# Kernel optimization log

Hardware: AMD Instinct MI355X
Metric: run time of the kernel (lower is better)

The kernel has to match this reference:

```python
import jax, jax.numpy as jnp
import numpy as np

ALPHA = 0.2  # LeakyReLU negative slope
NEG_INF = -1.0e12


def setup_inputs() -> dict:
    key = jax.random.key(0)
    ks = jax.random.split(key, 8)
    N, F, D, H, M, Q = 4096, 512, 64, 4, 2, 128
    x = jax.random.normal(ks[0], (N, F), dtype=jnp.float32)
    adj = jax.random.randint(ks[1], (M, N, N), 0, 2, dtype=jnp.int32)
    W = jax.random.normal(ks[2], (H, F, D), dtype=jnp.float32) * 0.07
    a1 = jax.random.normal(ks[3], (H, D), dtype=jnp.float32) * 0.15
    a2 = jax.random.normal(ks[4], (H, D), dtype=jnp.float32) * 0.15
    Ws = jax.random.normal(ks[5], (H * D, Q), dtype=jnp.float32) * 0.1
    bs = jax.random.normal(ks[6], (1, Q), dtype=jnp.float32) * 0.1
    q_sem = jax.random.normal(ks[7], (Q, 1), dtype=jnp.float32) * 0.15
    return {"x": x, "adj": adj, "W": W, "a1": a1, "a2": a2,
            "Ws": Ws, "bs": bs, "q_sem": q_sem}


def reference(x, adj, W, a1, a2, Ws, bs, q_sem):
    N = x.shape[0]
    # Wh is identical across meta-paths (dropout disabled / eval mode)
    Wh = jnp.einsum('nf,hfd->hnd', x, W)            # [H,N,D]
    s1 = jnp.einsum('hnd,hd->hn', Wh, a1)           # Wh @ a[:D]
    s2 = jnp.einsum('hnd,hd->hn', Wh, a2)           # Wh @ a[D:]

    def metapath(adj_m):
        # e[h,i,j] = leaky_relu(s1[h,i] + s2[h,j]); mask by adjacency
        e = jax.nn.leaky_relu(s1[:, :, None] + s2[:, None, :], negative_slope=ALPHA)
        e = jnp.where(adj_m[None, :, :] > 0, e, NEG_INF)
        att = jax.nn.softmax(e, axis=2)             # softmax over neighbors (dim=1 in torch [N,N])
        h = jax.nn.elu(jnp.einsum('hnm,hmd->hnd', att, Wh))
        return jnp.transpose(h, (1, 0, 2)).reshape(N, -1)  # concat heads -> [N, H*D]

    Z = jax.vmap(metapath)(adj)                     # [M, N, H*D]
    z = jnp.transpose(Z, (1, 0, 2))                 # [N, M, H*D]

    # Semantic attention (faithful to original, incl. softmax over dim=1 of [M,1])
    Whs = jnp.tanh(jnp.einsum('nmf,fq->nmq', z, Ws) + bs)   # [N,M,Q]
    w = jnp.einsum('nmq,qo->nmo', Whs, q_sem).mean(0)        # [M,1]
    beta = jax.nn.softmax(w, axis=1)                          # [M,1]
    return (beta[None, :, :] * z).sum(axis=1)                 # [N, H*D]
```

## Files before the change

### kernel.cpp

```cpp
#include <hip/hip_runtime.h>
#include <hip/hip_fp16.h>
#include <stdint.h>

#define NN 4096
#define FF 512
#define DD 64
#define HH 4
#define MM 2
#define LOG2E 1.44269504088896340736f
#define ALPHA_LR 0.2f

typedef float f32x4 __attribute__((ext_vector_type(4)));
typedef _Float16 f16x8 __attribute__((ext_vector_type(8)));
typedef _Float16 f16x2 __attribute__((ext_vector_type(2)));
typedef unsigned short u16x2 __attribute__((ext_vector_type(2)));

extern "C" __device__ _Float16 __ocml_exp2_f16(_Float16);

union H4 { ushort4 u; _Float16 h[4]; };
union W8 { f16x8 v; uint32_t w[4]; f16x2 p[4]; };

__device__ inline float fast_exp2(float x) { return __builtin_amdgcn_exp2f(x); }
__device__ inline float fast_rcp(float x) { return __builtin_amdgcn_rcpf(x); }
__device__ inline f32x4 mfma16(f16x8 a, f16x8 b, f32x4 c) {
    return __builtin_amdgcn_mfma_f32_16x16x32_f16(a, b, c, 0, 0, 0);
}
__device__ inline uint32_t enc_f32(float f) {
    uint32_t u = __float_as_uint(f);
    return (u & 0x80000000u) ? ~u : (u | 0x80000000u);
}
__device__ inline float dec_f32(uint32_t k) {
    uint32_t u = (k & 0x80000000u) ? (k ^ 0x80000000u) : ~k;
    return __uint_as_float(u);
}
__device__ inline f16x2 msk01(uint32_t V, int k) {
    uint32_t w = (V >> (2 * k)) & 0x00010001u;
    u16x2 m = __builtin_bit_cast(u16x2, w) * (u16x2){0x3C00, 0x3C00};
    return __builtin_bit_cast(f16x2, m);
}
__device__ inline f16x2 pkmax(f16x2 a, f16x2 b) {
#if __has_builtin(__builtin_elementwise_max)
    return __builtin_elementwise_max(a, b);
#else
    return (f16x2){a[0] > b[0] ? a[0] : b[0], a[1] > b[1] ? a[1] : b[1]};
#endif
}

__global__ __launch_bounds__(256) void k_prep(const int* __restrict__ adj,
                                              const float* __restrict__ W,
                                              _Float16* __restrict__ wt,
                                              unsigned long long* __restrict__ bitsT,
                                              uint32_t* __restrict__ m4a) {
    const int bid = blockIdx.x;
    if (bid < 2048) {
        const long long total = (long long)MM * NN * NN;
        const long long stride = 2048LL * 256;
        long long tid = (long long)bid * 256 + threadIdx.x;
        for (long long e = tid; e < total; e += stride) {
            unsigned long long msk = __ballot(adj[e] != 0);
            if ((threadIdx.x & 63) == 0) {
                long long q = e >> 6;
                int m  = (int)(q >> 18);
                int rem = (int)(q & 262143);
                int i  = rem >> 6;
                int jw = rem & 63;
                bitsT[((size_t)m * 64 + jw) * NN + i] = msk;
            }
        }
    } else {
        int t = (bid - 2048) * 256 + threadIdx.x;
        if (t < HH) m4a[t] = 0u;
        int c = t >> 9, f = t & 511;
        int h = c >> 6, d = c & 63;
        wt[t] = (_Float16)W[(h * FF + f) * DD + d];
    }
}

__global__ __launch_bounds__(512) void k_wh(const float* __restrict__ x,
                                            const _Float16* __restrict__ wt,
                                            const float* __restrict__ a1,
                                            const float* __restrict__ a2,
                                            _Float16* __restrict__ whT,
                                            float* __restrict__ s1L,
                                            _Float16* __restrict__ s2h,
                                            uint32_t* __restrict__ m4a) {
    __shared__ float sred[8][2][16];
    const int wave = threadIdx.x >> 6;
    const int h    = wave & 3;
    const int th   = wave >> 2;
    const int lane = threadIdx.x & 63;
    const int iL   = lane & 15;
    const int quad = lane >> 4;
    const int i0   = blockIdx.x * 16;

    f32x4 acc[2];
    acc[0] = (f32x4){0.f, 0.f, 0.f, 0.f};
    acc[1] = (f32x4){0.f, 0.f, 0.f, 0.f};

    const float* arow = x + (size_t)(i0 + iL) * FF + quad * 8;
    const _Float16* bbase = wt + (size_t)(h * 64 + th * 32 + iL) * FF + quad * 8;

    for (int kc = 0; kc < FF; kc += 32) {
        f32x4 xa = *(const f32x4*)(arow + kc);
        f32x4 xb = *(const f32x4*)(arow + kc + 4);
        f16x8 a;
        #pragma unroll
        for (int r = 0; r < 4; ++r) {
            a[r]     = (_Float16)xa[r];
            a[4 + r] = (_Float16)xb[r];
        }
        #pragma unroll
        for (int u = 0; u < 2; ++u) {
            f16x8 b = *(const f16x8*)(bbase + (size_t)(16 * u) * FF + kc);
            acc[u] = mfma16(a, b, acc[u]);
        }
    }
    #pragma unroll
    for (int u = 0; u < 2; ++u) {
        H4 o;
        #pragma unroll
        for (int r = 0; r < 4; ++r) o.h[r] = (_Float16)acc[u][r];
        *(ushort4*)(whT + (size_t)(h * 64 + th * 32 + 16 * u + iL) * NN + i0 + quad * 4) = o.u;
    }

    const float a1v0 = a1[h * 64 + th * 32 + iL];
    const float a1v1 = a1[h * 64 + th * 32 + 16 + iL];
    const float a2v0 = a2[h * 64 + th * 32 + iL];
    const float a2v1 = a2[h * 64 + th * 32 + 16 + iL];
    #pragma unroll
    for (int r = 0; r < 4; ++r) {
        float p1 = acc[0][r] * a1v0 + acc[1][r] * a1v1;
        float p2 = acc[0][r] * a2v0 + acc[1][r] * a2v1;
        #pragma unroll
        for (int off = 1; off < 16; off <<= 1) {
            p1 += __shfl_xor(p1, off);
            p2 += __shfl_xor(p2, off);
        }
        if (iL == 0) {
            sred[wave][0][quad * 4 + r] = p1;
            sred[wave][1][quad * 4 + r] = p2;
        }
    }
    __syncthreads();
    if (threadIdx.x < 64) {
        int h2  = threadIdx.x >> 4;
        int idx = threadIdx.x & 15;
        float s1 = sred[h2][0][idx] + sred[h2 + 4][0][idx];
        float s2 = sred[h2][1][idx] + sred[h2 + 4][1][idx];
        float s2l = s2 * LOG2E;
        s1L[h2 * NN + i0 + idx] = s1 * LOG2E;
        s2h[h2 * NN + i0 + idx] = (_Float16)s2l;
        float mx = s2l;
        #pragma unroll
        for (int off = 1; off < 16; off <<= 1) mx = fmaxf(mx, __shfl_xor(mx, off));
        if (idx == 0) atomicMax(m4a + h2, enc_f32(mx));
    }
}

__global__ __launch_bounds__(512, 1) void k_attn(const _Float16* __restrict__ whT,
                                                 const float* __restrict__ s1L,
                                                 const _Float16* __restrict__ s2h,
                                                 const uint32_t* __restrict__ m4a,
                                                 const unsigned long long* __restrict__ bitsT,
                                                 float* __restrict__ out) {
    __shared__ __align__(16) float xr[8][MM][4][16][16];
    __shared__ __align__(16) float dr[8][MM][16];

    const int tid  = threadIdx.x;
    const int wave = tid >> 6;
    const int lane = tid & 63;
    const int iL   = lane & 15;
    const int quad = lane >> 4;
    const int h    = blockIdx.x & 3;
    const int i0   = (blockIdx.x >> 2) * 64;

    const float m4 = dec_f32(m4a[h]);
    f16x2 A2[4], B2[4];
    #pragma unroll
    for (int s = 0; s < 4; ++s) {
        float s1i = s1L[h * NN + i0 + 16 * s + iL];
        float vv  = s1i + m4;
        float cii = fmaxf(vv, ALPHA_LR * vv);
        _Float16 a = (_Float16)(s1i - cii);
        _Float16 b = (_Float16)(ALPHA_LR * s1i - cii);
        A2[s] = (f16x2){a, a};
        B2[s] = (f16x2){b, b};
    }
    const f16x2 al2 = (f16x2){(_Float16)ALPHA_LR, (_Float16)ALPHA_LR};

    f32x4 acc[4][MM][4];
    f32x4 accD[4][MM];
    #pragma unroll
    for (int s = 0; s < 4; ++s)
        #pragma unroll
        for (int m = 0; m < MM; ++m) {
            accD[s][m] = (f32x4){0.f, 0.f, 0.f, 0.f};
            #pragma unroll
            for (int t = 0; t < 4; ++t) acc[s][m][t] = (f32x4){0.f, 0.f, 0.f, 0.f};
        }

    f16x8 bones;
    #pragma unroll
    for (int e = 0; e < 8; ++e) bones[e] = (_Float16)1.0f;

    const _Float16* s2row = s2h + h * NN;
    const _Float16* brow = whT + (size_t)(h * 64 + iL) * NN;
    const int qshift = quad * 8;
    const int jbase = wave * 512;

    const unsigned long long* pB[MM][4];
    #pragma unroll
    for (int m = 0; m < MM; ++m)
        #pragma unroll
        for (int s = 0; s < 4; ++s)
            pB[m][s] = bitsT + (size_t)m * 64 * NN + i0 + 16 * s + iL;

    #pragma unroll 1
    for (int it = 0; it < 8; ++it) {
        const int jc = jbase + it * 64;
        const int jw = jc >> 6;
        unsigned long long bm[MM][4];
        #pragma unroll
        for (int m = 0; m < MM; ++m)
            #pragma unroll
            for (int s = 0; s < 4; ++s)
                bm[m][s] = pB[m][s][(size_t)jw * NN];

        #pragma unroll
        for (int half = 0; half < 2; ++half) {
            const int jb = jc + 32 * half;
            f16x8 bfr[4];
            #pragma unroll
            for (int t = 0; t < 4; ++t)
                bfr[t] = *(const f16x8*)(brow + (size_t)(16 * t) * NN + jb + qshift);

            const W8 s2v = *(const W8*)(s2row + jb + qshift);
            const int shft = 32 * half + qshift;

            #pragma unroll
            for (int s = 0; s < 4; ++s) {
                uint32_t rs0 = (uint32_t)(bm[0][s] >> shft) & 0xFFu;
                uint32_t rs1 = (uint32_t)(bm[1][s] >> shft) & 0xFFu;
                uint32_t V0 = rs0 | (rs0 << 15);
                uint32_t V1 = rs1 | (rs1 << 15);
                W8 a0, a1v;
                #pragma unroll
                for (int k = 0; k < 4; ++k) {
                    f16x2 z = s2v.p[k] + A2[s];
                    f16x2 l = al2 * s2v.p[k] + B2[s];
                    f16x2 mx = pkmax(z, l);
                    f16x2 p = (f16x2){__ocml_exp2_f16(mx[0]), __ocml_exp2_f16(mx[1])};
                    a0.p[k]  = p * msk01(V0, k);
                    a1v.p[k] = p * msk01(V1, k);
                }
                #pragma unroll
                for (int t = 0; t < 4; ++t) {
                    acc[s][0][t] = mfma16(a0.v, bfr[t], acc[s][0][t]);
                    acc[s][1][t] = mfma16(a1v.v, bfr[t], acc[s][1][t]);
                }
                accD[s][0] = mfma16(a0.v, bones, accD[s][0]);
                accD[s][1] = mfma16(a1v.v, bones, accD[s][1]);
            }
        }
    }

    #pragma unroll
    for (int s = 0; s < 4; ++s) {
        __syncthreads();
        #pragma unroll
        for (int m = 0; m < MM; ++m) {
            #pragma unroll
            for (int t = 0; t < 4; ++t)
                *(f32x4*)&xr[wave][m][t][iL][quad * 4] = acc[s][m][t];
            if (iL == 0) *(f32x4*)&dr[wave][m][quad * 4] = accD[s][m];
        }
        __syncthreads();
        if (wave < 4) {
            const int t = wave;
            f32x4 n0 = (f32x4){0.f, 0.f, 0.f, 0.f};
            f32x4 n1 = (f32x4){0.f, 0.f, 0.f, 0.f};
            f32x4 d0 = (f32x4){0.f, 0.f, 0.f, 0.f};
            f32x4 d1 = (f32x4){0.f, 0.f, 0.f, 0.f};
            #pragma unroll
            for (int sl = 0; sl < 8; ++sl) {
                n0 += *(const f32x4*)&xr[sl][0][t][iL][quad * 4];
                n1 += *(const f32x4*)&xr[sl][1][t][iL][quad * 4];
                d0 += *(const f32x4*)&dr[sl][0][quad * 4];
                d1 += *(const f32x4*)&dr[sl][1][quad * 4];
            }
            const int i0s = i0 + 16 * s;
            #pragma unroll
            for (int r = 0; r < 4; ++r) {
                float v0 = n0[r] * fast_rcp(d0[r]);
                float v1 = n1[r] * fast_rcp(d1[r]);
                float e0 = v0 > 0.f ? v0 : (fast_exp2(v0 * LOG2E) - 1.f);
                float e1 = v1 > 0.f ? v1 : (fast_exp2(v1 * LOG2E) - 1.f);
                out[(size_t)(i0s + quad * 4 + r) * (HH * DD) + h * 64 + 16 * t + iL] = e0 + e1;
            }
        }
    }
}

extern "C" void kernel_launch(void* const* d_in, const int* in_sizes, int n_in,
                              void* d_out, int out_size, void* d_ws, size_t ws_size,
                              hipStream_t stream) {
    const float* x   = (const float*)d_in[0];
    const int*   adj = (const int*)d_in[1];
    const float* W   = (const float*)d_in[2];
    const float* a1  = (const float*)d_in[3];
    const float* a2  = (const float*)d_in[4];
    float* out = (float*)d_out;

    char* ws = (char*)d_ws;
    _Float16* wt   = (_Float16*)(ws);
    _Float16* whT  = (_Float16*)(ws + 262144);
    float*    s1L  = (float*)(ws + 2359296);
    _Float16* s2h  = (_Float16*)(ws + 2424832);
    uint32_t* m4a  = (uint32_t*)(ws + 2457600);
    unsigned long long* bitsT = (unsigned long long*)(ws + 2490368);

    hipLaunchKernelGGL(k_prep, dim3(2560), dim3(256), 0, stream,
                       adj, W, wt, bitsT, m4a);
    hipLaunchKernelGGL(k_wh, dim3(256), dim3(512), 0, stream,
                       x, wt, a1, a2, whT, s1L, s2h, m4a);
    hipLaunchKernelGGL(k_attn, dim3(256), dim3(512), 0, stream,
                       whT, s1L, s2h, m4a, bitsT, out);
}
```

Baseline: 272.0 us.

## Software-pipeline loads and replace denominator MFMAs with fdot2 reductions

The main attention loop is restructured with double-buffered registers, so the adjacency bitmask, Wh^T fragments and s2 values for the next half-tile are loaded while the current half-tile is computed. The row-sum denominator is no longer computed with extra MFMA instructions against a ones vector. Instead each lane accumulates it with packed fdot2 in fp32 and reduces across quads with shuffles at the end. This removes two MFMAs per sub-tile and hides global load latency, at the cost of more live registers, which may reduce occupancy. Loop-tail prefetches use wrapped indices, so they read in-bounds but unused data.

```diff
diff --git a/kernel.cpp b/kernel.cpp
--- a/kernel.cpp
+++ b/kernel.cpp
@@ -24,6 +24,13 @@
 __device__ inline float fast_rcp(float x) { return __builtin_amdgcn_rcpf(x); }
 __device__ inline f32x4 mfma16(f16x8 a, f16x8 b, f32x4 c) {
     return __builtin_amdgcn_mfma_f32_16x16x32_f16(a, b, c, 0, 0, 0);
+}
+__device__ inline float fdot2_(f16x2 a, f16x2 b, float c) {
+#if __has_builtin(__builtin_amdgcn_fdot2)
+    return __builtin_amdgcn_fdot2(a, b, c, false);
+#else
+    return c + (float)a[0] * (float)b[0] + (float)a[1] * (float)b[1];
+#endif
 }
 __device__ inline uint32_t enc_f32(float f) {
     uint32_t u = __float_as_uint(f);
@@ -187,82 +194,98 @@
         B2[s] = (f16x2){b, b};
     }
     const f16x2 al2 = (f16x2){(_Float16)ALPHA_LR, (_Float16)ALPHA_LR};
+    const f16x2 one2 = (f16x2){(_Float16)1.0f, (_Float16)1.0f};
 
     f32x4 acc[4][MM][4];
-    f32x4 accD[4][MM];
+    float dden[4][MM];
     #pragma unroll
     for (int s = 0; s < 4; ++s)
         #pragma unroll
         for (int m = 0; m < MM; ++m) {
-            accD[s][m] = (f32x4){0.f, 0.f, 0.f, 0.f};
+            dden[s][m] = 0.f;
             #pragma unroll
             for (int t = 0; t < 4; ++t) acc[s][m][t] = (f32x4){0.f, 0.f, 0.f, 0.f};
         }
-
-    f16x8 bones;
-    #pragma unroll
-    for (int e = 0; e < 8; ++e) bones[e] = (_Float16)1.0f;
 
     const _Float16* s2row = s2h + h * NN;
     const _Float16* brow = whT + (size_t)(h * 64 + iL) * NN;
     const int qshift = quad * 8;
     const int jbase = wave * 512;
 
-    const unsigned long long* pB[MM][4];
-    #pragma unroll
-    for (int m = 0; m < MM; ++m)
-        #pragma unroll
-        for (int s = 0; s < 4; ++s)
-            pB[m][s] = bitsT + (size_t)m * 64 * NN + i0 + 16 * s + iL;
-
+#define LOADS(BFR, S2V, ITV, HALF)                                              \
+    do {                                                                        \
+        const int jb_ = ((jbase + (ITV) * 64 + 32 * (HALF)) & (NN - 1)) + qshift; \
+        _Pragma("unroll")                                                       \
+        for (int t = 0; t < 4; ++t)                                             \
+            BFR[t] = *(const f16x8*)(brow + (size_t)(16 * t) * NN + jb_);       \
+        S2V.v = *(const f16x8*)(s2row + jb_);                                   \
+    } while (0)
+
+#define BMLOAD(BM, ITV)                                                         \
+    do {                                                                        \
+        const int jw_ = ((jbase + (ITV) * 64) >> 6) & 63;                       \
+        const unsigned long long* bp_ = bitsT + (size_t)jw_ * NN + i0 + iL;     \
+        _Pragma("unroll")                                                       \
+        for (int m = 0; m < MM; ++m)                                            \
+            _Pragma("unroll")                                                   \
+            for (int s = 0; s < 4; ++s)                                         \
+                BM[m][s] = bp_[(size_t)m * 64 * NN + 16 * s];                   \
+    } while (0)
+
+#define COMPUTE(HALF, BM, BFR, S2V)                                             \
+    do {                                                                        \
+        const int shft_ = 32 * (HALF) + qshift;                                 \
+        _Pragma("unroll")                                                       \
+        for (int s = 0; s < 4; ++s) {                                           \
+            uint32_t rs0 = (uint32_t)(BM[0][s] >> shft_) & 0xFFu;               \
+            uint32_t rs1 = (uint32_t)(BM[1][s] >> shft_) & 0xFFu;               \
+            uint32_t V0 = rs0 | (rs0 << 15);                                    \
+            uint32_t V1 = rs1 | (rs1 << 15);                                    \
+            W8 a0, a1v;                                                         \
+            _Pragma("unroll")                                                   \
+            for (int k = 0; k < 4; ++k) {                                       \
+                f16x2 z = S2V.p[k] + A2[s];                   \
+                f16x2 l = al2 * S2V.p[k] + B2[s];             \
+                f16x2 mx = pkmax(z, l);                       \
+                f16x2 p = (f16x2){__ocml_exp2_f16(mx[0]), __ocml_exp2_f16(mx[1])}; \
+                a0.p[k]  = p * msk01(V0, k);                                    \
+                a1v.p[k] = p * msk01(V1, k);                                    \
+            }                                                                   \
+            _Pragma("unroll")                                                   \
+            for (int t = 0; t < 4; ++t) {                                       \
+                acc[s][0][t] = mfma16(a0.v, BFR[t], acc[s][0][t]);              \
+                acc[s][1][t] = mfma16(a1v.v, BFR[t], acc[s][1][t]);             \
+            }                                                                   \
+            _Pragma("unroll")                                                   \
+            for (int k = 0; k < 4; ++k) {                                       \
+                dden[s][0] = fdot2_(a0.p[k], one2, dden[s][0]);                 \
+                dden[s][1] = fdot2_(a1v.p[k], one2, dden[s][1]);                \
+            }                                                                   \
+        }                                                                       \
+    } while (0)
+
+    unsigned long long bmA[MM][4], bmB[MM][4];
+    f16x8 bfrA[4], bfrB[4];
+    W8 s2vA, s2vB;
+
+    BMLOAD(bmA, 0);
+    LOADS(bfrA, s2vA, 0, 0);
     #pragma unroll 1
-    for (int it = 0; it < 8; ++it) {
-        const int jc = jbase + it * 64;
-        const int jw = jc >> 6;
-        unsigned long long bm[MM][4];
-        #pragma unroll
-        for (int m = 0; m < MM; ++m)
-            #pragma unroll
-            for (int s = 0; s < 4; ++s)
-                bm[m][s] = pB[m][s][(size_t)jw * NN];
-
-        #pragma unroll
-        for (int half = 0; half < 2; ++half) {
-            const int jb = jc + 32 * half;
-            f16x8 bfr[4];
-            #pragma unroll
-            for (int t = 0; t < 4; ++t)
-                bfr[t] = *(const f16x8*)(brow + (size_t)(16 * t) * NN + jb + qshift);
-
-            const W8 s2v = *(const W8*)(s2row + jb + qshift);
-            const int shft = 32 * half + qshift;
-
-            #pragma unroll
-            for (int s = 0; s < 4; ++s) {
-                uint32_t rs0 = (uint32_t)(bm[0][s] >> shft) & 0xFFu;
-                uint32_t rs1 = (uint32_t)(bm[1][s] >> shft) & 0xFFu;
-                uint32_t V0 = rs0 | (rs0 << 15);
-                uint32_t V1 = rs1 | (rs1 << 15);
-                W8 a0, a1v;
-                #pragma unroll
-                for (int k = 0; k < 4; ++k) {
-                    f16x2 z = s2v.p[k] + A2[s];
-                    f16x2 l = al2 * s2v.p[k] + B2[s];
-                    f16x2 mx = pkmax(z, l);
-                    f16x2 p = (f16x2){__ocml_exp2_f16(mx[0]), __ocml_exp2_f16(mx[1])};
-                    a0.p[k]  = p * msk01(V0, k);
-                    a1v.p[k] = p * msk01(V1, k);
-                }
-                #pragma unroll
-                for (int t = 0; t < 4; ++t) {
-                    acc[s][0][t] = mfma16(a0.v, bfr[t], acc[s][0][t]);
-                    acc[s][1][t] = mfma16(a1v.v, bfr[t], acc[s][1][t]);
-                }
-                accD[s][0] = mfma16(a0.v, bones, accD[s][0]);
-                accD[s][1] = mfma16(a1v.v, bones, accD[s][1]);
-            }
-        }
-    }
+    for (int it = 0; it < 8; it += 2) {
+        LOADS(bfrB, s2vB, it, 1);
+        BMLOAD(bmB, it + 1);
+        COMPUTE(0, bmA, bfrA, s2vA);
+        LOADS(bfrA, s2vA, it + 1, 0);
+        COMPUTE(1, bmA, bfrB, s2vB);
+        LOADS(bfrB, s2vB, it + 1, 1);
+        BMLOAD(bmA, it + 2);
+        COMPUTE(0, bmB, bfrA, s2vA);
+        LOADS(bfrA, s2vA, it + 2, 0);
+        COMPUTE(1, bmB, bfrB, s2vB);
+    }
+#undef LOADS
+#undef BMLOAD
+#undef COMPUTE
 
     #pragma unroll
     for (int s = 0; s < 4; ++s) {
@@ -272,7 +295,16 @@
             #pragma unroll
             for (int t = 0; t < 4; ++t)
                 *(f32x4*)&xr[wave][m][t][iL][quad * 4] = acc[s][m][t];
-            if (iL == 0) *(f32x4*)&dr[wave][m][quad * 4] = accD[s][m];
+        }
+        {
+            float d0v = dden[s][0];
+            float d1v = dden[s][1];
+            d0v += __shfl_xor(d0v, 16); d0v += __shfl_xor(d0v, 32);
+            d1v += __shfl_xor(d1v, 16); d1v += __shfl_xor(d1v, 32);
+            if (quad == 0) {
+                dr[wave][0][iL] = d0v;
+                dr[wave][1][iL] = d1v;
+            }
         }
         __syncthreads();
         if (wave < 4) {
```

Result: slower. 288.1 us (+5.9%).

## Double-buffer Wh tiles into LDS via async global_load_lds in attention kernel

Applied to the files above, without the earlier changes.

Each wave now prefetches its next 64-column chunk of the transposed Wh matrix into a per-wave double buffer in LDS with global_load_lds. It then reads MFMA B fragments from LDS using an XOR-swizzled layout instead of loading them directly from global memory. The s2 values for both halves are loaded up front. The goal is to overlap global latency with the exp/MFMA work. In exchange it adds 128KB of LDS, reused by the epilogue through a union, and a full vmcnt wait per iteration.

```diff
diff --git a/kernel.cpp b/kernel.cpp
--- a/kernel.cpp
+++ b/kernel.cpp
@@ -45,6 +45,11 @@
     return (f16x2){a[0] > b[0] ? a[0] : b[0], a[1] > b[1] ? a[1] : b[1]};
 #endif
 }
+
+#define GLOAD_LDS(G, L)                                                     \
+    __builtin_amdgcn_global_load_lds(                                       \
+        (const __attribute__((address_space(1))) void*)(G),                 \
+        (__attribute__((address_space(3))) void*)(L), 16, 0, 0)
 
 __global__ __launch_bounds__(256) void k_prep(const int* __restrict__ adj,
                                               const float* __restrict__ W,
@@ -163,8 +168,14 @@
                                                  const uint32_t* __restrict__ m4a,
                                                  const unsigned long long* __restrict__ bitsT,
                                                  float* __restrict__ out) {
-    __shared__ __align__(16) float xr[8][MM][4][16][16];
-    __shared__ __align__(16) float dr[8][MM][16];
+    union __align__(16) Smem {
+        _Float16 stage[8][2][4096];
+        struct {
+            float xr[8][MM][4][16][16];
+            float dr[8][MM][16];
+        } epi;
+    };
+    __shared__ Smem sm;
 
     const int tid  = threadIdx.x;
     const int wave = tid >> 6;
@@ -204,16 +215,36 @@
     for (int e = 0; e < 8; ++e) bones[e] = (_Float16)1.0f;
 
     const _Float16* s2row = s2h + h * NN;
-    const _Float16* brow = whT + (size_t)(h * 64 + iL) * NN;
     const int qshift = quad * 8;
     const int jbase = wave * 512;
 
+    const _Float16* stBase = whT
+        + (size_t)(h * 64 + (lane >> 3)) * NN
+        + (((lane & 7) ^ ((lane >> 3) & 7)) << 3);
+    const int x3 = iL & 7;
+    int rdOff[2];
+    #pragma unroll
+    for (int hf = 0; hf < 2; ++hf)
+        rdOff[hf] = (iL << 7) + ((((hf << 2) + quad) ^ x3) << 4);
+
+    _Float16* cur = &sm.stage[wave][0][0];
+    _Float16* nxt = &sm.stage[wave][1][0];
+
     const unsigned long long* pB[MM][4];
     #pragma unroll
     for (int m = 0; m < MM; ++m)
         #pragma unroll
         for (int s = 0; s < 4; ++s)
             pB[m][s] = bitsT + (size_t)m * 64 * NN + i0 + 16 * s + iL;
+
+    {
+        const _Float16* src = stBase + jbase;
+        #pragma unroll
+        for (int k = 0; k < 8; ++k)
+            GLOAD_LDS(src + (size_t)(k * 8) * NN, cur + k * 512);
+    }
+    asm volatile("s_waitcnt vmcnt(0)" ::: "memory");
+    __builtin_amdgcn_sched_barrier(0);
 
     #pragma unroll 1
     for (int it = 0; it < 8; ++it) {
@@ -225,17 +256,26 @@
             #pragma unroll
             for (int s = 0; s < 4; ++s)
                 bm[m][s] = pB[m][s][(size_t)jw * NN];
+        W8 s2vh[2];
+        s2vh[0].v = *(const f16x8*)(s2row + jc + qshift);
+        s2vh[1].v = *(const f16x8*)(s2row + jc + 32 + qshift);
+
+        __builtin_amdgcn_sched_barrier(0);
+        if (it < 7) {
+            const _Float16* src = stBase + (jc + 64);
+            #pragma unroll
+            for (int k = 0; k < 8; ++k)
+                GLOAD_LDS(src + (size_t)(k * 8) * NN, nxt + k * 512);
+        }
+        __builtin_amdgcn_sched_barrier(0);
 
         #pragma unroll
         for (int half = 0; half < 2; ++half) {
-            const int jb = jc + 32 * half;
+            const int shft = 32 * half + qshift;
             f16x8 bfr[4];
             #pragma unroll
             for (int t = 0; t < 4; ++t)
-                bfr[t] = *(const f16x8*)(brow + (size_t)(16 * t) * NN + jb + qshift);
-
-            const W8 s2v = *(const W8*)(s2row + jb + qshift);
-            const int shft = 32 * half + qshift;
+                bfr[t] = *(const f16x8*)((const char*)cur + (t << 11) + rdOff[half]);
 
             #pragma unroll
             for (int s = 0; s < 4; ++s) {
@@ -246,8 +286,8 @@
                 W8 a0, a1v;
                 #pragma unroll
                 for (int k = 0; k < 4; ++k) {
-                    f16x2 z = s2v.p[k] + A2[s];
-                    f16x2 l = al2 * s2v.p[k] + B2[s];
+                    f16x2 z = s2vh[half].p[k] + A2[s];
+                    f16x2 l = al2 * s2vh[half].p[k] + B2[s];
                     f16x2 mx = pkmax(z, l);
                     f16x2 p = (f16x2){__ocml_exp2_f16(mx[0]), __ocml_exp2_f16(mx[1])};
                     a0.p[k]  = p * msk01(V0, k);
@@ -262,6 +302,10 @@
                 accD[s][1] = mfma16(a1v.v, bones, accD[s][1]);
             }
         }
+
+        asm volatile("s_waitcnt vmcnt(0)" ::: "memory");
+        __builtin_amdgcn_sched_barrier(0);
+        _Float16* tmp = cur; cur = nxt; nxt = tmp;
     }
 
     #pragma unroll
@@ -271,8 +315,8 @@
         for (int m = 0; m < MM; ++m) {
             #pragma unroll
             for (int t = 0; t < 4; ++t)
-                *(f32x4*)&xr[wave][m][t][iL][quad * 4] = acc[s][m][t];
-            if (iL == 0) *(f32x4*)&dr[wave][m][quad * 4] = accD[s][m];
+                *(f32x4*)&sm.epi.xr[wave][m][t][iL][quad * 4] = acc[s][m][t];
+            if (iL == 0) *(f32x4*)&sm.epi.dr[wave][m][quad * 4] = accD[s][m];
         }
         __syncthreads();
         if (wave < 4) {
@@ -283,10 +327,10 @@
             f32x4 d1 = (f32x4){0.f, 0.f, 0.f, 0.f};
             #pragma unroll
             for (int sl = 0; sl < 8; ++sl) {
-                n0 += *(const f32x4*)&xr[sl][0][t][iL][quad * 4];
-                n1 += *(const f32x4*)&xr[sl][1][t][iL][quad * 4];
-                d0 += *(const f32x4*)&dr[sl][0][quad * 4];
-                d1 += *(const f32x4*)&dr[sl][1][quad * 4];
+                n0 += *(const f32x4*)&sm.epi.xr[sl][0][t][iL][quad * 4];
+                n1 += *(const f32x4*)&sm.epi.xr[sl][1][t][iL][quad * 4];
+                d0 += *(const f32x4*)&sm.epi.dr[sl][0][quad * 4];
+                d1 += *(const f32x4*)&sm.epi.dr[sl][1][quad * 4];
             }
             const int i0s = i0 + 16 * s;
             #pragma unroll
```

Result: no change. 270.9 us (-0.4%).
